# Kernel tuning notes

Measured on AMD Instinct MI355X. Metric: run time of the kernel, lower is better.

Reference implementation:

```python
import jax, jax.numpy as jnp
import numpy as np

NUM_HEADS = 16
D_MODEL = 2048
DUPLICATES = 4
DEPTH = D_MODEL // NUM_HEADS  # 128
KV_HEADS = NUM_HEADS // DUPLICATES  # 4


def rope(x):
    # x: (b, s, d); RoPE over first 2*(d//2) dims (d even here), as in source
    b, s, d = x.shape
    dim = d // 2
    inv_freq = (10000.0 ** (-jnp.arange(0, dim, dtype=jnp.float32) / dim)).astype(x.dtype)
    pos = jnp.arange(s, dtype=x.dtype)[None, :, None]  # (1, s, 1)
    freqs = pos * inv_freq  # (1, s, dim)
    cos, sin = jnp.cos(freqs), jnp.sin(freqs)
    x1, x2 = x[..., :dim], x[..., dim:]
    return jnp.concatenate([x1 * cos - x2 * sin, x2 * cos + x1 * sin], axis=-1)


def setup_inputs() -> dict:
    key = jax.random.key(0)
    ks = jax.random.split(key, 6)
    b, s = 2, 2048
    x = jax.random.normal(ks[0], (b, s, D_MODEL), dtype=jnp.float32)
    mask = jnp.ones((b, 1, s, s), dtype=bool)
    std = 0.02
    Wq = jax.random.normal(ks[1], (D_MODEL, D_MODEL), dtype=jnp.float32) * std
    Wk = jax.random.normal(ks[2], (D_MODEL, D_MODEL // DUPLICATES), dtype=jnp.float32) * std
    Wv = jax.random.normal(ks[3], (D_MODEL, D_MODEL // DUPLICATES), dtype=jnp.float32) * std
    Wo = jax.random.normal(ks[4], (D_MODEL, D_MODEL), dtype=jnp.float32) * std
    bo = jnp.zeros((1, 1, D_MODEL), dtype=jnp.float32)
    return {"x": x, "mask": mask, "Wq": Wq, "Wk": Wk, "Wv": Wv, "Wo": Wo, "bo": bo}


def reference(x, mask, Wq, Wk, Wv, Wo, bo):
    b, s, d = x.shape
    # QKV projections; RoPE applied on full projected vectors (as in source)
    q = rope(x @ Wq)          # (b, s, d_model)
    k = rope(x @ Wk)          # (b, s, d_model/dup)
    v = x @ Wv                # (b, s, d_model/dup)
    # split heads
    q = q.reshape(b, s, NUM_HEADS, DEPTH).transpose(0, 2, 1, 3)     # (b, H, s, depth)
    k = k.reshape(b, s, KV_HEADS, DEPTH).transpose(0, 2, 1, 3)      # (b, Hkv, s, depth)
    v = v.reshape(b, s, KV_HEADS, DEPTH).transpose(0, 2, 1, 3)
    # GQA repeat (jnp.repeat on head axis, matching source)
    k = jnp.repeat(k, DUPLICATES, axis=1)                            # (b, H, s, depth)
    v = jnp.repeat(v, DUPLICATES, axis=1)
    # scaled dot-product attention (chunking in source is a pure partition of q; math identical)
    logits = jnp.einsum('bhqd,bhkd->bhqk', q, k) / jnp.sqrt(jnp.asarray(DEPTH, x.dtype))
    logits = jnp.where(mask, logits, jnp.asarray(-1e9, x.dtype))
    attn = jax.nn.softmax(logits, axis=-1)
    out = jnp.einsum('bhqk,bhkd->bhqd', attn, v)                     # (b, H, s, depth)
    out = out.transpose(0, 2, 1, 3).reshape(b, s, d)
    return out @ Wo + bo
```

## Files before the change

kernel.cpp:

```cpp
#include <hip/hip_runtime.h>
#include <hip/hip_bf16.h>
#include <stdint.h>

#define NHEADS 16
#define KVHEADS 4
#define DEPTH 128
#define SEQ 2048
#define DM 2048
#define NQKV 3072
#define SCALE 0.08838834764831845f
#define LOG2E 1.4426950408889634f
#define QSCL (SCALE * LOG2E)

using u16 = unsigned short;
using u32 = unsigned int;
using u64 = unsigned long long;
using bf16x8 = __attribute__((ext_vector_type(8))) __bf16;
using f32x4  = __attribute__((ext_vector_type(4))) float;
using f32x16 = __attribute__((ext_vector_type(16))) float;
using u32x4  = __attribute__((ext_vector_type(4))) u32;

__device__ __forceinline__ u16 bits(float f) {
  return __builtin_bit_cast(u16, (__bf16)f);
}
__device__ __forceinline__ u32 pk2(float a, float b) {
  return (u32)bits(a) | ((u32)bits(b) << 16);
}
__device__ __forceinline__ float ex2(float x) {
#if __has_builtin(__builtin_amdgcn_exp2f)
  return __builtin_amdgcn_exp2f(x);
#else
  return exp2f(x);
#endif
}

__device__ __forceinline__ void gll16(const void* g, void* l) {
  __builtin_amdgcn_global_load_lds((const __attribute__((address_space(1))) void*)g,
                                   (__attribute__((address_space(3))) void*)l, 16, 0, 0);
}


__global__ void k_cvt_x(const float4* __restrict__ x, u16* __restrict__ o, int n4) {
  int i = blockIdx.x * 256 + threadIdx.x;
  if (i >= n4) return;
  float4 v = x[i];
  u64 pk = (u64)bits(v.x) | ((u64)bits(v.y) << 16) | ((u64)bits(v.z) << 32) | ((u64)bits(v.w) << 48);
  reinterpret_cast<u64*>(o)[i] = pk;
}

__global__ void k_transpose_w(const float* __restrict__ in, u16* __restrict__ out, int K, int N) {
  __shared__ float tile[32][33];
  int n0 = blockIdx.x * 32, k0 = blockIdx.y * 32;
  int tx = threadIdx.x, ty = threadIdx.y;
  for (int i = 0; i < 4; i++) tile[ty + i * 8][tx] = in[(size_t)(k0 + ty + i * 8) * N + n0 + tx];
  __syncthreads();
  for (int i = 0; i < 4; i++)
    out[(size_t)(n0 + ty + i * 8) * K + k0 + tx] = bits(tile[tx][ty + i * 8]);
}

__global__ void k_trig(float2* __restrict__ tab) {
  int idx = blockIdx.x * 256 + threadIdx.x;
  int s = idx >> 10, j = idx & 1023;
  float inv = expf((float)j * (-9.210340371976184f / 1024.f));
  float f = (float)s * inv;
  float sv, cv;
  sincosf(f, &sv, &cv);
  tab[idx] = make_float2(cv, sv);
}

__global__ void k_rope_q(const float* __restrict__ qkv, const float2* __restrict__ tab,
                         u16* __restrict__ Qh) {
  int idx = blockIdx.x * 256 + threadIdx.x;
  int col = idx & 2047;
  int row = idx >> 11;
  int s = row & 2047;
  const float* base = qkv + (size_t)row * NQKV;
  float v = base[col], out;
  if (col < 1024) {
    float2 cs = tab[s * 1024 + col];
    out = v * cs.x - base[col + 1024] * cs.y;
  } else {
    int j = col - 1024;
    float2 cs = tab[s * 1024 + j];
    out = v * cs.x + base[col - 1024] * cs.y;
  }
  int h = col >> 7, d = col & 127;
  Qh[(((size_t)(row >> 11) * NHEADS + h) * SEQ + s) * DEPTH + d] = bits(out * QSCL);
}

__global__ void k_rope_k(const float* __restrict__ qkv, const float2* __restrict__ tab,
                         u16* __restrict__ Kh) {
  int idx = blockIdx.x * 256 + threadIdx.x;
  int col = idx & 511;
  int row = idx >> 9;
  int s = row & 2047;
  const float* base = qkv + (size_t)row * NQKV + 2048;
  float v = base[col], out;
  if (col < 256) {
    float2 cs = tab[s * 1024 + col * 4];
    out = v * cs.x - base[col + 256] * cs.y;
  } else {
    int j = col - 256;
    float2 cs = tab[s * 1024 + j * 4];
    out = v * cs.x + base[col - 256] * cs.y;
  }
  int h = col >> 7, d = col & 127;
  Kh[(((size_t)(row >> 11) * KVHEADS + h) * SEQ + s) * DEPTH + d] = bits(out);
}

__global__ void k_transpose_v(const float* __restrict__ qkv, u16* __restrict__ Vt) {
  __shared__ float tile[32][33];
  int gy = blockIdx.y;
  int d0 = (gy & 3) * 32, kvh = (gy >> 2) & 3, b = gy >> 4;
  int s0 = blockIdx.x * 32;
  int tx = threadIdx.x, ty = threadIdx.y;
  const float* base = qkv + (size_t)b * SEQ * NQKV + 2560 + kvh * 128 + d0;
  for (int i = 0; i < 4; i++)
    tile[ty + i * 8][tx] = base[(size_t)(s0 + ty + i * 8) * NQKV + tx];
  __syncthreads();
  u16* obase = Vt + (((size_t)b * KVHEADS + kvh) * DEPTH + d0) * SEQ;
  for (int i = 0; i < 4; i++)
    obase[(size_t)(ty + i * 8) * SEQ + s0 + tx] = bits(tile[tx][ty + i * 8]);
}


#define GBAR __builtin_amdgcn_s_barrier()

#define GSTAGE(GBASE, LHALF, KT, ROWB) do {                                   \
  _Pragma("unroll") for (int i_ = 0; i_ < 2; i_++) {                          \
    int rl_ = (l >> 3) + w * 8 + i_ * 64;                                     \
    int cs_ = (l & 7) ^ ((rl_ & 4) >> 1);                                     \
    gll16((GBASE) + (size_t)((ROWB) + rl_) * K + (KT) * 64 + cs_ * 8,         \
          (char*)(LHALF) + w * 1024 + i_ * 8192);                             \
  }                                                                           \
} while (0)

#define LDA8(DB, MH) do {                                                     \
  const char* pa_ = (const char*)lA[DB][wm];                                  \
  _Pragma("unroll") for (int mi_ = 0; mi_ < 4; mi_++)                         \
  _Pragma("unroll") for (int kk_ = 0; kk_ < 2; kk_++) {                       \
    int row_ = (MH) * 64 + mi_ * 16 + lr;                                     \
    af[mi_ * 2 + kk_] = *(const bf16x8*)(pa_ + row_ * 128 +                   \
        (((kk_ * 4 + lg) ^ ((row_ & 4) >> 1)) * 16));                         \
  }                                                                           \
} while (0)

#define LDB4(DB, NH) do {                                                     \
  const char* pb_ = (const char*)lB[DB][wn >> 1];                             \
  _Pragma("unroll") for (int ni_ = 0; ni_ < 2; ni_++)                         \
  _Pragma("unroll") for (int kk_ = 0; kk_ < 2; kk_++) {                       \
    int row_ = (wn & 1) * 64 + (NH) * 32 + ni_ * 16 + lr;                     \
    bfr[ni_ * 2 + kk_] = *(const bf16x8*)(pb_ + row_ * 128 +                  \
        (((kk_ * 4 + lg) ^ ((row_ & 4) >> 1)) * 16));                         \
  }                                                                           \
} while (0)

#define PHASE_MFMA(MH, NH) do {                                               \
  __builtin_amdgcn_s_setprio(1);                                             \
  _Pragma("unroll") for (int mi_ = 0; mi_ < 4; mi_++)                         \
  _Pragma("unroll") for (int ni_ = 0; ni_ < 2; ni_++)                         \
  _Pragma("unroll") for (int kk_ = 0; kk_ < 2; kk_++)                         \
    acc[MH][NH][mi_][ni_] = __builtin_amdgcn_mfma_f32_16x16x32_bf16(          \
        af[mi_ * 2 + kk_], bfr[ni_ * 2 + kk_], acc[MH][NH][mi_][ni_], 0, 0, 0); \
  __builtin_amdgcn_s_setprio(0);                                             \
} while (0)

__global__ __launch_bounds__(512, 2) void k_gemm256(const u16* __restrict__ A,
                                                    const u16* __restrict__ B,
                                                    float* __restrict__ C, int M, int N, int K,
                                                    const float* __restrict__ bias) {
  __shared__ __align__(16) u16 lA[2][2][128 * 64];
  __shared__ __align__(16) u16 lB[2][2][128 * 64];
  int nt = N >> 8;
  int nwg = gridDim.x;
  int bid = blockIdx.x;
  int swz = (bid & 7) * (nwg >> 3) + (bid >> 3);
  int bm = swz / nt, bn = swz % nt;
  int tid = threadIdx.x;
  int w = tid >> 6, l = tid & 63;
  int lr = l & 15, lg = l >> 4;
  int wm = w >> 2, wn = w & 3;
  const u16* Abase = A + (size_t)(bm * 256) * K;
  const u16* Bbase = B + (size_t)(bn * 256) * K;
  int NT = K >> 6;

  f32x4 acc[2][2][4][2] = {};

  GSTAGE(Abase, lA[0][0], 0, 0);
  GSTAGE(Abase, lA[0][1], 0, 128);
  GSTAGE(Bbase, lB[0][0], 0, 0);
  GSTAGE(Bbase, lB[0][1], 0, 128);
  GSTAGE(Abase, lA[1][0], 1, 0);
  GSTAGE(Abase, lA[1][1], 1, 128);
  asm volatile("s_waitcnt vmcnt(4)" ::: "memory");
  GBAR;

  for (int j = 0; j < (NT >> 1); j++) {
    int kt1 = 2 * j + 1;
    int kt2 = (2 * j + 2) & (NT - 1);
    int kt3 = (2 * j + 3) & (NT - 1);
    bf16x8 af[8];
    bf16x8 bfr[4];
    LDA8(0, 0);
    LDB4(0, 0);
    GSTAGE(Bbase, lB[1][0], kt1, 0);
    GSTAGE(Bbase, lB[1][1], kt1, 128);
    GBAR;
    PHASE_MFMA(0, 0);
    GBAR;
    LDB4(0, 1);
    GBAR;
    PHASE_MFMA(0, 1);
    GBAR;
    LDA8(0, 1);
    GBAR;
    PHASE_MFMA(1, 1);
    GBAR;
    LDB4(0, 0);
    GSTAGE(Abase, lA[0][0], kt2, 0);
    GSTAGE(Abase, lA[0][1], kt2, 128);
    asm volatile("s_waitcnt vmcnt(4)" ::: "memory");
    GBAR;
    PHASE_MFMA(1, 0);
    GBAR;
    LDA8(1, 0);
    LDB4(1, 0);
    GSTAGE(Bbase, lB[0][0], kt2, 0);
    GSTAGE(Bbase, lB[0][1], kt2, 128);
    GBAR;
    PHASE_MFMA(0, 0);
    GBAR;
    LDB4(1, 1);
    GBAR;
    PHASE_MFMA(0, 1);
    GBAR;
    LDA8(1, 1);
    GBAR;
    PHASE_MFMA(1, 1);
    GBAR;
    LDB4(1, 0);
    GSTAGE(Abase, lA[1][0], kt3, 0);
    GSTAGE(Abase, lA[1][1], kt3, 128);
    asm volatile("s_waitcnt vmcnt(4)" ::: "memory");
    GBAR;
    PHASE_MFMA(1, 0);
    GBAR;
  }
  asm volatile("s_waitcnt vmcnt(0)" ::: "memory");

  int r0 = bm * 256 + wm * 128, c0 = bn * 256 + wn * 64;
#pragma unroll
  for (int mh = 0; mh < 2; mh++)
#pragma unroll
    for (int mi = 0; mi < 4; mi++)
#pragma unroll
      for (int nh = 0; nh < 2; nh++)
#pragma unroll
        for (int ni = 0; ni < 2; ni++) {
          int col = c0 + nh * 32 + ni * 16 + lr;
          float bv = bias ? bias[col] : 0.f;
#pragma unroll
          for (int r = 0; r < 4; r++) {
            int row = r0 + mh * 64 + mi * 16 + lg * 4 + r;
            C[(size_t)row * N + col] = acc[mh][nh][mi][ni][r] + bv;
          }
        }
}

__global__ __launch_bounds__(256, 2) void k_attn(const u16* __restrict__ Qh,
                                                 const u16* __restrict__ Kh,
                                                 const u16* __restrict__ Vt,
                                                 u16* __restrict__ Ao) {
  __shared__ u16 lK[2][64 * 128];
  __shared__ u16 lV[2][128 * 64];
  __shared__ float lsc[4][32];

  int bid = blockIdx.x;
  int swz = (bid & 7) * 64 + (bid >> 3);
  int qt = swz & 15;
  int hd = (swz >> 4) & 3, kvh = (swz >> 6) & 3, b = swz >> 8;
  int h = kvh * 4 + hd;

  int tid = threadIdx.x;
  int w = tid >> 6, l = tid & 63;
  int hi = l >> 5;
  int q32 = l & 31;

  const u16* Kb = Kh + ((size_t)b * KVHEADS + kvh) * SEQ * DEPTH;
  const u16* Vb = Vt + ((size_t)b * KVHEADS + kvh) * DEPTH * SEQ;

  const u16* Qp = Qh + (((size_t)(b * NHEADS + h) * SEQ) + qt * 128 + w * 32 + q32) * DEPTH + hi * 8;
  bf16x8 qf[8];
#pragma unroll
  for (int ds = 0; ds < 8; ds++)
    qf[ds] = *reinterpret_cast<const bf16x8*>(Qp + ds * 16);

  f32x16 oacc[4] = {};
  float mrun = -INFINITY, lrun = 0.f;
  bool lo = (l < 32);

  {
#pragma unroll
    for (int i = 0; i < 4; i++) {
      int g = (w * 4 + i) * 64 + l;
      int kv = g >> 4, c = g & 15;
      gll16(Kb + (size_t)kv * DEPTH + ((c ^ (kv & 15)) << 3), (char*)lK[0] + (w * 4 + i) * 1024);
      int d = g >> 3, cv = g & 7;
      gll16(Vb + (size_t)d * SEQ + ((cv ^ (d & 7)) << 3), (char*)lV[0] + (w * 4 + i) * 1024);
    }
  }
  __syncthreads();

  int cur = 0;
  for (int t = 0; t < 32; t++) {
    if (t < 31) {
      int kv0 = (t + 1) * 64;
#pragma unroll
      for (int i = 0; i < 4; i++) {
        int g = (w * 4 + i) * 64 + l;
        int kv = g >> 4, c = g & 15;
        gll16(Kb + (size_t)(kv0 + kv) * DEPTH + ((c ^ (kv & 15)) << 3),
              (char*)lK[cur ^ 1] + (w * 4 + i) * 1024);
        int d = g >> 3, cv = g & 7;
        gll16(Vb + (size_t)d * SEQ + kv0 + ((cv ^ (d & 7)) << 3),
              (char*)lV[cur ^ 1] + (w * 4 + i) * 1024);
      }
    }

    const u16* lk = lK[cur];
    f32x16 sa[2] = {};
    __builtin_amdgcn_s_setprio(1);
#pragma unroll
    for (int ds = 0; ds < 8; ds++) {
#pragma unroll
      for (int a = 0; a < 2; a++) {
        int kv = a * 32 + q32;
        bf16x8 kf = *reinterpret_cast<const bf16x8*>(
            &lk[kv * DEPTH + (((ds * 2 + hi) ^ (kv & 15)) << 3)]);
        sa[a] = __builtin_amdgcn_mfma_f32_32x32x16_bf16(kf, qf[ds], sa[a], 0, 0, 0);
      }
    }
    __builtin_amdgcn_s_setprio(0);

    float mx[16];
#pragma unroll
    for (int r = 0; r < 16; r++) mx[r] = fmaxf(sa[0][r], sa[1][r]);
#pragma unroll
    for (int s = 8; s > 0; s >>= 1)
#pragma unroll
      for (int r = 0; r < 16; r++)
        if (r < s) mx[r] = fmaxf(mx[r], mx[r + s]);
    float pmax = fmaxf(mx[0], __shfl_xor(mx[0], 32, 64));
    if (!__all(pmax - mrun <= 11.54f)) {
      float mnew = fmaxf(mrun, pmax);
      float al = ex2(mrun - mnew);
      mrun = mnew;
      lrun *= al;
#pragma unroll
      for (int db = 0; db < 4; db++)
#pragma unroll
        for (int r = 0; r < 16; r++) oacc[db][r] *= al;
    }
    float ss[16];
#pragma unroll
    for (int r = 0; r < 16; r++) {
      float p0 = ex2(sa[0][r] - mrun);
      float p1 = ex2(sa[1][r] - mrun);
      sa[0][r] = p0;
      sa[1][r] = p1;
      ss[r] = p0 + p1;
    }
#pragma unroll
    for (int s = 8; s > 0; s >>= 1)
#pragma unroll
      for (int r = 0; r < 16; r++)
        if (r < s) ss[r] += ss[r + s];
    lrun += ss[0] + __shfl_xor(ss[0], 32, 64);

    const u16* lv = lV[cur];
#pragma unroll
    for (int a = 0; a < 2; a++) {
#pragma unroll
      for (int js = 0; js < 2; js++) {
        int base = js * 8;
        u32 A0 = pk2(sa[a][base + 0], sa[a][base + 1]);
        u32 A1 = pk2(sa[a][base + 2], sa[a][base + 3]);
        u32 B0 = pk2(sa[a][base + 4], sa[a][base + 5]);
        u32 B1 = pk2(sa[a][base + 6], sa[a][base + 7]);
        asm volatile("v_permlane32_swap_b32 %0, %1" : "+v"(A0), "+v"(B0));
        asm volatile("v_permlane32_swap_b32 %0, %1" : "+v"(A1), "+v"(B1));
        u32x4 tw;
        tw.x = A0;
        tw.y = A1;
        tw.z = B0;
        tw.w = B1;
        bf16x8 pa = __builtin_bit_cast(bf16x8, tw);
        int ks = a * 2 + js;
        __builtin_amdgcn_s_setprio(1);
#pragma unroll
        for (int db = 0; db < 4; db++) {
          int d = db * 32 + q32;
          bf16x8 vf = *reinterpret_cast<const bf16x8*>(
              &lv[d * 64 + (((ks * 2 + hi) ^ (d & 7)) << 3)]);
          oacc[db] = __builtin_amdgcn_mfma_f32_32x32x16_bf16(pa, vf, oacc[db], 0, 0, 0);
        }
        __builtin_amdgcn_s_setprio(0);
      }
    }

    __syncthreads();
    cur ^= 1;
  }

  if (lo) lsc[w][q32] = 1.f / lrun;
  int q0 = qt * 128 + w * 32;
  u16* ob = Ao + (size_t)b * SEQ * DM + (size_t)h * DEPTH;
#pragma unroll
  for (int db = 0; db < 4; db++)
#pragma unroll
    for (int r = 0; r < 16; r++) {
      int row = (r & 3) + 8 * (r >> 2) + 4 * hi;
      ob[(size_t)(q0 + row) * DM + db * 32 + q32] = bits(oacc[db][r] * lsc[w][row]);
    }
}


extern "C" void kernel_launch(void* const* d_in, const int* in_sizes, int n_in,
                              void* d_out, int out_size, void* d_ws, size_t ws_size,
                              hipStream_t stream) {
  const float* x  = (const float*)d_in[0];
  const float* Wq = (const float*)d_in[2];
  const float* Wk = (const float*)d_in[3];
  const float* Wv = (const float*)d_in[4];
  const float* Wo = (const float*)d_in[5];
  const float* bo = (const float*)d_in[6];
  float* out = (float*)d_out;
  char* ws = (char*)d_ws;

  const size_t OFF_XB  = 0;
  const size_t OFF_WT  = 16777216;
  const size_t OFF_WOT = 29360128;
  const size_t OFF_TAB = 37748736;
  const size_t OFF_QKV = 54525952;
  const size_t OFF_QH  = 104857600;
  const size_t OFF_KH  = 121634816;
  const size_t OFF_VT  = 125829120;
  const size_t OFF_AO  = OFF_QKV;

  u16*    xb    = (u16*)(ws + OFF_XB);
  u16*    wqkvT = (u16*)(ws + OFF_WT);
  u16*    woT   = (u16*)(ws + OFF_WOT);
  float2* tab   = (float2*)(ws + OFF_TAB);
  float*  qkv   = (float*)(ws + OFF_QKV);
  u16*    Qhh   = (u16*)(ws + OFF_QH);
  u16*    Khh   = (u16*)(ws + OFF_KH);
  u16*    Vtt   = (u16*)(ws + OFF_VT);
  u16*    Ao    = (u16*)(ws + OFF_AO);

  dim3 tb(32, 8);
  k_cvt_x<<<8192, 256, 0, stream>>>((const float4*)x, xb, 2097152);
  k_transpose_w<<<dim3(64, 64), tb, 0, stream>>>(Wq, wqkvT, 2048, 2048);
  k_transpose_w<<<dim3(16, 64), tb, 0, stream>>>(Wk, wqkvT + (size_t)2048 * 2048, 2048, 512);
  k_transpose_w<<<dim3(16, 64), tb, 0, stream>>>(Wv, wqkvT + (size_t)2560 * 2048, 2048, 512);
  k_transpose_w<<<dim3(64, 64), tb, 0, stream>>>(Wo, woT, 2048, 2048);
  k_trig<<<8192, 256, 0, stream>>>(tab);
  k_gemm256<<<192, 512, 0, stream>>>(xb, wqkvT, qkv, 4096, 3072, 2048, nullptr);
  k_rope_q<<<32768, 256, 0, stream>>>(qkv, tab, Qhh);
  k_rope_k<<<8192, 256, 0, stream>>>(qkv, tab, Khh);
  k_transpose_v<<<dim3(64, 32), tb, 0, stream>>>(qkv, Vtt);
  k_attn<<<512, 256, 0, stream>>>(Qhh, Khh, Vtt, Ao);
  k_gemm256<<<128, 512, 0, stream>>>(Ao, woT, out, 4096, 2048, 2048, bo);
}
```

Before: 411.9 us.

## Fuse RoPE, head split and V transpose into QKV GEMM epilogue

The Wq/Wk columns are permuted when the weights are prepared so that each RoPE pair lands in the same thread's accumulators. The QKV GEMM epilogue can then apply RoPE and scaling and write bf16 Q/K heads and transposed V directly. This removes the fp32 QKV intermediate round trip and three separate elementwise and transpose kernels. It also merges three weight-transpose launches into one, changes the K LDS swizzle from kv&15 to kv&7, and simplifies the softmax max and sum reductions in attention. The epilogue stores are more scattered and less coalesced in exchange.

```diff
diff --git a/kernel.cpp b/kernel.cpp
--- a/kernel.cpp
+++ b/kernel.cpp
@@ -48,6 +48,34 @@
   reinterpret_cast<u64*>(o)[i] = pk;
 }
 
+__global__ void k_prep_wqkv(const float* __restrict__ Wq, const float* __restrict__ Wk,
+                            const float* __restrict__ Wv, u16* __restrict__ out) {
+  __shared__ float tile[32][33];
+  int c0 = blockIdx.x * 32, k0 = blockIdx.y * 32;
+  int tx = threadIdx.x, ty = threadIdx.y;
+  const float* src;
+  int scol, sN;
+  if (c0 < 2048) { src = Wq; scol = c0; sN = 2048; }
+  else if (c0 < 2560) { src = Wk; scol = c0 - 2048; sN = 512; }
+  else { src = Wv; scol = c0 - 2560; sN = 512; }
+  for (int i = 0; i < 4; i++)
+    tile[ty + i * 8][tx] = src[(size_t)(k0 + ty + i * 8) * sN + scol + tx];
+  __syncthreads();
+  for (int i = 0; i < 4; i++) {
+    int c = c0 + ty + i * 8;
+    int N;
+    if (c < 2048) {
+      N = ((c & 1023) >> 4) * 32 + ((c >= 1024) ? 16 : 0) + (c & 15);
+    } else if (c < 2560) {
+      int cc = c - 2048;
+      N = 2048 + ((cc & 255) >> 4) * 32 + ((cc >= 256) ? 16 : 0) + (cc & 15);
+    } else {
+      N = c;
+    }
+    out[(size_t)N * 2048 + k0 + tx] = bits(tile[tx][ty + i * 8]);
+  }
+}
+
 __global__ void k_transpose_w(const float* __restrict__ in, u16* __restrict__ out, int K, int N) {
   __shared__ float tile[32][33];
   int n0 = blockIdx.x * 32, k0 = blockIdx.y * 32;
@@ -66,61 +94,6 @@
   float sv, cv;
   sincosf(f, &sv, &cv);
   tab[idx] = make_float2(cv, sv);
-}
-
-__global__ void k_rope_q(const float* __restrict__ qkv, const float2* __restrict__ tab,
-                         u16* __restrict__ Qh) {
-  int idx = blockIdx.x * 256 + threadIdx.x;
-  int col = idx & 2047;
-  int row = idx >> 11;
-  int s = row & 2047;
-  const float* base = qkv + (size_t)row * NQKV;
-  float v = base[col], out;
-  if (col < 1024) {
-    float2 cs = tab[s * 1024 + col];
-    out = v * cs.x - base[col + 1024] * cs.y;
-  } else {
-    int j = col - 1024;
-    float2 cs = tab[s * 1024 + j];
-    out = v * cs.x + base[col - 1024] * cs.y;
-  }
-  int h = col >> 7, d = col & 127;
-  Qh[(((size_t)(row >> 11) * NHEADS + h) * SEQ + s) * DEPTH + d] = bits(out * QSCL);
-}
-
-__global__ void k_rope_k(const float* __restrict__ qkv, const float2* __restrict__ tab,
-                         u16* __restrict__ Kh) {
-  int idx = blockIdx.x * 256 + threadIdx.x;
-  int col = idx & 511;
-  int row = idx >> 9;
-  int s = row & 2047;
-  const float* base = qkv + (size_t)row * NQKV + 2048;
-  float v = base[col], out;
-  if (col < 256) {
-    float2 cs = tab[s * 1024 + col * 4];
-    out = v * cs.x - base[col + 256] * cs.y;
-  } else {
-    int j = col - 256;
-    float2 cs = tab[s * 1024 + j * 4];
-    out = v * cs.x + base[col - 256] * cs.y;
-  }
-  int h = col >> 7, d = col & 127;
-  Kh[(((size_t)(row >> 11) * KVHEADS + h) * SEQ + s) * DEPTH + d] = bits(out);
-}
-
-__global__ void k_transpose_v(const float* __restrict__ qkv, u16* __restrict__ Vt) {
-  __shared__ float tile[32][33];
-  int gy = blockIdx.y;
-  int d0 = (gy & 3) * 32, kvh = (gy >> 2) & 3, b = gy >> 4;
-  int s0 = blockIdx.x * 32;
-  int tx = threadIdx.x, ty = threadIdx.y;
-  const float* base = qkv + (size_t)b * SEQ * NQKV + 2560 + kvh * 128 + d0;
-  for (int i = 0; i < 4; i++)
-    tile[ty + i * 8][tx] = base[(size_t)(s0 + ty + i * 8) * NQKV + tx];
-  __syncthreads();
-  u16* obase = Vt + (((size_t)b * KVHEADS + kvh) * DEPTH + d0) * SEQ;
-  for (int i = 0; i < 4; i++)
-    obase[(size_t)(ty + i * 8) * SEQ + s0 + tx] = bits(tile[tx][ty + i * 8]);
 }
 
 
@@ -165,10 +138,14 @@
   __builtin_amdgcn_s_setprio(0);                                             \
 } while (0)
 
+template <int MODE>
 __global__ __launch_bounds__(512, 2) void k_gemm256(const u16* __restrict__ A,
                                                     const u16* __restrict__ B,
                                                     float* __restrict__ C, int M, int N, int K,
-                                                    const float* __restrict__ bias) {
+                                                    const float* __restrict__ bias,
+                                                    const float2* __restrict__ tab,
+                                                    u16* __restrict__ Qh, u16* __restrict__ Kh,
+                                                    u16* __restrict__ Vt) {
   __shared__ __align__(16) u16 lA[2][2][128 * 64];
   __shared__ __align__(16) u16 lB[2][2][128 * 64];
   int nt = N >> 8;
@@ -248,23 +225,74 @@
   }
   asm volatile("s_waitcnt vmcnt(0)" ::: "memory");
 
-  int r0 = bm * 256 + wm * 128, c0 = bn * 256 + wn * 64;
-#pragma unroll
-  for (int mh = 0; mh < 2; mh++)
-#pragma unroll
-    for (int mi = 0; mi < 4; mi++)
-#pragma unroll
-      for (int nh = 0; nh < 2; nh++)
-#pragma unroll
-        for (int ni = 0; ni < 2; ni++) {
-          int col = c0 + nh * 32 + ni * 16 + lr;
-          float bv = bias ? bias[col] : 0.f;
-#pragma unroll
-          for (int r = 0; r < 4; r++) {
-            int row = r0 + mh * 64 + mi * 16 + lg * 4 + r;
-            C[(size_t)row * N + col] = acc[mh][nh][mi][ni][r] + bv;
+  if constexpr (MODE == 0) {
+    int r0 = bm * 256 + wm * 128, c0 = bn * 256 + wn * 64;
+#pragma unroll
+    for (int mh = 0; mh < 2; mh++)
+#pragma unroll
+      for (int mi = 0; mi < 4; mi++)
+#pragma unroll
+        for (int nh = 0; nh < 2; nh++)
+#pragma unroll
+          for (int ni = 0; ni < 2; ni++) {
+            int col = c0 + nh * 32 + ni * 16 + lr;
+            float bv = bias ? bias[col] : 0.f;
+#pragma unroll
+            for (int r = 0; r < 4; r++) {
+              int row = r0 + mh * 64 + mi * 16 + lg * 4 + r;
+              C[(size_t)row * N + col] = acc[mh][nh][mi][ni][r] + bv;
+            }
+          }
+  } else {
+    int c0 = bn * 256 + wn * 64;
+#pragma unroll
+    for (int mh = 0; mh < 2; mh++)
+#pragma unroll
+      for (int mi = 0; mi < 4; mi++) {
+        int rowb = bm * 256 + wm * 128 + mh * 64 + mi * 16 + lg * 4;
+        int b = rowb >> 11, s = rowb & 2047;
+#pragma unroll
+        for (int nh = 0; nh < 2; nh++) {
+          int col = c0 + nh * 32;
+          if (col < 2048) {
+            int m = ((col >> 5) << 4) + lr;
+            int h = m >> 7, d = m & 127;
+            size_t o0 = (((size_t)(b * NHEADS + h) * SEQ) + s) * DEPTH + d;
+#pragma unroll
+            for (int r = 0; r < 4; r++) {
+              float2 cs = tab[(size_t)(s + r) * 1024 + m];
+              float v0 = acc[mh][nh][mi][0][r], v1 = acc[mh][nh][mi][1][r];
+              Qh[o0 + (size_t)r * DEPTH] = bits((v0 * cs.x - v1 * cs.y) * QSCL);
+              Qh[o0 + (size_t)8 * SEQ * DEPTH + (size_t)r * DEPTH] =
+                  bits((v1 * cs.x + v0 * cs.y) * QSCL);
+            }
+          } else if (col < 2560) {
+            int mk = (((col - 2048) >> 5) << 4) + lr;
+            int h = mk >> 7, d = mk & 127;
+            size_t o0 = (((size_t)(b * KVHEADS + h) * SEQ) + s) * DEPTH + d;
+#pragma unroll
+            for (int r = 0; r < 4; r++) {
+              float2 cs = tab[(size_t)(s + r) * 1024 + 4 * mk];
+              float v0 = acc[mh][nh][mi][0][r], v1 = acc[mh][nh][mi][1][r];
+              Kh[o0 + (size_t)r * DEPTH] = bits(v0 * cs.x - v1 * cs.y);
+              Kh[o0 + (size_t)2 * SEQ * DEPTH + (size_t)r * DEPTH] =
+                  bits(v1 * cs.x + v0 * cs.y);
+            }
+          } else {
+#pragma unroll
+            for (int ni = 0; ni < 2; ni++) {
+              int c = col + ni * 16 + lr - 2560;
+              int kvh = c >> 7, d = c & 127;
+              f32x4 v = acc[mh][nh][mi][ni];
+              u64 pk = (u64)bits(v[0]) | ((u64)bits(v[1]) << 16) |
+                       ((u64)bits(v[2]) << 32) | ((u64)bits(v[3]) << 48);
+              *reinterpret_cast<u64*>(
+                  &Vt[(((size_t)(b * KVHEADS + kvh) * DEPTH) + d) * SEQ + s]) = pk;
+            }
           }
         }
+      }
+  }
 }
 
 __global__ __launch_bounds__(256, 2) void k_attn(const u16* __restrict__ Qh,
@@ -304,7 +332,7 @@
     for (int i = 0; i < 4; i++) {
       int g = (w * 4 + i) * 64 + l;
       int kv = g >> 4, c = g & 15;
-      gll16(Kb + (size_t)kv * DEPTH + ((c ^ (kv & 15)) << 3), (char*)lK[0] + (w * 4 + i) * 1024);
+      gll16(Kb + (size_t)kv * DEPTH + ((c ^ (kv & 7)) << 3), (char*)lK[0] + (w * 4 + i) * 1024);
       int d = g >> 3, cv = g & 7;
       gll16(Vb + (size_t)d * SEQ + ((cv ^ (d & 7)) << 3), (char*)lV[0] + (w * 4 + i) * 1024);
     }
@@ -319,7 +347,7 @@
       for (int i = 0; i < 4; i++) {
         int g = (w * 4 + i) * 64 + l;
         int kv = g >> 4, c = g & 15;
-        gll16(Kb + (size_t)(kv0 + kv) * DEPTH + ((c ^ (kv & 15)) << 3),
+        gll16(Kb + (size_t)(kv0 + kv) * DEPTH + ((c ^ (kv & 7)) << 3),
               (char*)lK[cur ^ 1] + (w * 4 + i) * 1024);
         int d = g >> 3, cv = g & 7;
         gll16(Vb + (size_t)d * SEQ + kv0 + ((cv ^ (d & 7)) << 3),
@@ -336,21 +364,18 @@
       for (int a = 0; a < 2; a++) {
         int kv = a * 32 + q32;
         bf16x8 kf = *reinterpret_cast<const bf16x8*>(
-            &lk[kv * DEPTH + (((ds * 2 + hi) ^ (kv & 15)) << 3)]);
+            &lk[kv * DEPTH + (((ds * 2 + hi) ^ (kv & 7)) << 3)]);
         sa[a] = __builtin_amdgcn_mfma_f32_32x32x16_bf16(kf, qf[ds], sa[a], 0, 0, 0);
       }
     }
     __builtin_amdgcn_s_setprio(0);
 
-    float mx[16];
-#pragma unroll
-    for (int r = 0; r < 16; r++) mx[r] = fmaxf(sa[0][r], sa[1][r]);
-#pragma unroll
-    for (int s = 8; s > 0; s >>= 1)
-#pragma unroll
-      for (int r = 0; r < 16; r++)
-        if (r < s) mx[r] = fmaxf(mx[r], mx[r + s]);
-    float pmax = fmaxf(mx[0], __shfl_xor(mx[0], 32, 64));
+    float pmax = sa[0][0];
+#pragma unroll
+    for (int r = 1; r < 16; r++) pmax = fmaxf(pmax, sa[0][r]);
+#pragma unroll
+    for (int r = 0; r < 16; r++) pmax = fmaxf(pmax, sa[1][r]);
+    pmax = fmaxf(pmax, __shfl_xor(pmax, 32, 64));
     if (!__all(pmax - mrun <= 11.54f)) {
       float mnew = fmaxf(mrun, pmax);
       float al = ex2(mrun - mnew);
@@ -361,21 +386,17 @@
 #pragma unroll
         for (int r = 0; r < 16; r++) oacc[db][r] *= al;
     }
-    float ss[16];
-#pragma unroll
-    for (int r = 0; r < 16; r++) {
-      float p0 = ex2(sa[0][r] - mrun);
-      float p1 = ex2(sa[1][r] - mrun);
-      sa[0][r] = p0;
-      sa[1][r] = p1;
-      ss[r] = p0 + p1;
-    }
-#pragma unroll
-    for (int s = 8; s > 0; s >>= 1)
-#pragma unroll
-      for (int r = 0; r < 16; r++)
-        if (r < s) ss[r] += ss[r + s];
-    lrun += ss[0] + __shfl_xor(ss[0], 32, 64);
+    float ps = 0.f;
+#pragma unroll
+    for (int a = 0; a < 2; a++)
+#pragma unroll
+      for (int r = 0; r < 16; r++) {
+        float p = ex2(sa[a][r] - mrun);
+        sa[a][r] = p;
+        ps += p;
+      }
+    ps += __shfl_xor(ps, 32, 64);
+    lrun += ps;
 
     const u16* lv = lV[cur];
 #pragma unroll
@@ -441,17 +462,15 @@
   const size_t OFF_WT  = 16777216;
   const size_t OFF_WOT = 29360128;
   const size_t OFF_TAB = 37748736;
-  const size_t OFF_QKV = 54525952;
-  const size_t OFF_QH  = 104857600;
-  const size_t OFF_KH  = 121634816;
-  const size_t OFF_VT  = 125829120;
-  const size_t OFF_AO  = OFF_QKV;
+  const size_t OFF_QH  = 54525952;
+  const size_t OFF_KH  = 71303168;
+  const size_t OFF_VT  = 75497472;
+  const size_t OFF_AO  = 79691776;
 
   u16*    xb    = (u16*)(ws + OFF_XB);
   u16*    wqkvT = (u16*)(ws + OFF_WT);
   u16*    woT   = (u16*)(ws + OFF_WOT);
   float2* tab   = (float2*)(ws + OFF_TAB);
-  float*  qkv   = (float*)(ws + OFF_QKV);
   u16*    Qhh   = (u16*)(ws + OFF_QH);
   u16*    Khh   = (u16*)(ws + OFF_KH);
   u16*    Vtt   = (u16*)(ws + OFF_VT);
@@ -459,15 +478,12 @@
 
   dim3 tb(32, 8);
   k_cvt_x<<<8192, 256, 0, stream>>>((const float4*)x, xb, 2097152);
-  k_transpose_w<<<dim3(64, 64), tb, 0, stream>>>(Wq, wqkvT, 2048, 2048);
-  k_transpose_w<<<dim3(16, 64), tb, 0, stream>>>(Wk, wqkvT + (size_t)2048 * 2048, 2048, 512);
-  k_transpose_w<<<dim3(16, 64), tb, 0, stream>>>(Wv, wqkvT + (size_t)2560 * 2048, 2048, 512);
+  k_prep_wqkv<<<dim3(96, 64), tb, 0, stream>>>(Wq, Wk, Wv, wqkvT);
   k_transpose_w<<<dim3(64, 64), tb, 0, stream>>>(Wo, woT, 2048, 2048);
   k_trig<<<8192, 256, 0, stream>>>(tab);
-  k_gemm256<<<192, 512, 0, stream>>>(xb, wqkvT, qkv, 4096, 3072, 2048, nullptr);
-  k_rope_q<<<32768, 256, 0, stream>>>(qkv, tab, Qhh);
-  k_rope_k<<<8192, 256, 0, stream>>>(qkv, tab, Khh);
-  k_transpose_v<<<dim3(64, 32), tb, 0, stream>>>(qkv, Vtt);
+  k_gemm256<1><<<192, 512, 0, stream>>>(xb, wqkvT, nullptr, 4096, 3072, 2048, nullptr,
+                                        tab, Qhh, Khh, Vtt);
   k_attn<<<512, 256, 0, stream>>>(Qhh, Khh, Vtt, Ao);
-  k_gemm256<<<128, 512, 0, stream>>>(Ao, woT, out, 4096, 2048, 2048, bo);
-}
+  k_gemm256<0><<<128, 512, 0, stream>>>(Ao, woT, out, 4096, 2048, 2048, bo,
+                                        nullptr, nullptr, nullptr, nullptr);
+}
```

Measured after the change: 371.8 us. 9.7% less time.
